# Kernel tuning notes

Hardware: AMD Instinct MI355X
Metric: run time of the kernel (lower is better)

Reference implementation:

```python
import jax, jax.numpy as jnp
import numpy as np

DIM = 2048
NUM_HEADS = 4  # hardcoded in RetNext.__init__
HEAD_DIM = DIM // NUM_HEADS
B, T = 4, 4096


def setup_inputs() -> dict:
    key = jax.random.key(0)
    ks = jax.random.split(key, 7)
    s = 1.0 / np.sqrt(DIM)  # roughly nn.Linear init scale
    return {
        "x": jax.random.normal(ks[0], (B, T, DIM), dtype=jnp.float32),
        "Wk": jax.random.normal(ks[1], (DIM, DIM), dtype=jnp.float32) * s,
        "bk": jax.random.normal(ks[2], (DIM,), dtype=jnp.float32) * s,
        "Wq": jax.random.normal(ks[3], (DIM, DIM), dtype=jnp.float32) * s,
        "bq": jax.random.normal(ks[4], (DIM,), dtype=jnp.float32) * s,
        "Wv": jax.random.normal(ks[5], (DIM, DIM), dtype=jnp.float32) * s,
        "bv": jax.random.normal(ks[6], (DIM,), dtype=jnp.float32) * s,
    }


def reference(x, Wk, bk, Wq, bq, Wv, bv):
    bsz, seq_len, _ = x.shape
    # nn.Linear: y = x @ W.T + b
    k = x @ Wk.T + bk
    q = x @ Wq.T + bq
    v = x @ Wv.T + bv
    # (b, s, h, d) -> (b, h, s, d)
    k = k.reshape(bsz, seq_len, NUM_HEADS, HEAD_DIM).transpose(0, 2, 1, 3)
    q = q.reshape(bsz, seq_len, NUM_HEADS, HEAD_DIM).transpose(0, 2, 1, 3)
    v = v.reshape(bsz, seq_len, NUM_HEADS, HEAD_DIM).transpose(0, 2, 1, 3)
    # states = k^T @ v : (b, h, d, d)
    states = jnp.einsum("bhsd,bhse->bhde", k, v)
    # out = q @ states : (b, h, s, d) -- returned WITHOUT reshape, as in the source
    out = jnp.einsum("bhsd,bhde->bhse", q, states)
    return out
```

## Files before the change

### kernel.cpp

```cpp
#include <hip/hip_runtime.h>
#include <cstdint>
#include <cstddef>

typedef __bf16 bf16;
typedef bf16 bf16x8 __attribute__((ext_vector_type(8)));
typedef float f32x4 __attribute__((ext_vector_type(4)));
typedef unsigned short u16;
typedef u16 u16x4 __attribute__((ext_vector_type(4)));
typedef u16 u16x8 __attribute__((ext_vector_type(8)));

__device__ __forceinline__ u16 f2bf(float f) {
    uint32_t u = __builtin_bit_cast(uint32_t, f);
    u += 0x7FFFu + ((u >> 16) & 1u);
    return (u16)(u >> 16);
}

#define AS1C(p) ((const __attribute__((address_space(1))) uint32_t*)(p))
#define AS3(p)  ((__attribute__((address_space(3))) uint32_t*)(p))

__device__ __forceinline__ void gemm_core(const bf16* __restrict__ Ablk,
                                          const bf16* __restrict__ Btblk,
                                          int lda, int ldb, int K,
                                          f32x4 acc[4][4])
{
    __shared__ bf16 lA[4096];
    __shared__ bf16 lB[4096];

    const int tid  = threadIdx.x;
    const int wave = tid >> 6;
    const int lane = tid & 63;
    const int lrow = lane >> 2;
    const int kcol = (lane & 3) << 3;

    const bf16* ga0 = Ablk  + (size_t)(wave * 32 + lrow) * lda + kcol;
    const bf16* ga1 = ga0 + (size_t)16 * lda;
    const bf16* gb0 = Btblk + (size_t)(wave * 32 + lrow) * ldb + kcol;
    const bf16* gb1 = gb0 + (size_t)16 * ldb;
    bf16* la0 = &lA[wave * 1024];
    bf16* la1 = &lA[wave * 1024 + 512];
    bf16* lb0 = &lB[wave * 1024];
    bf16* lb1 = &lB[wave * 1024 + 512];

    const int wm    = (wave >> 1) * 64;
    const int wn    = (wave & 1) * 64;
    const int col16 = lane & 15;
    const int quad  = lane >> 4;
    const bf16* pa = &lA[(wm + col16) * 32 + quad * 8];
    const bf16* pb = &lB[(wn + col16) * 32 + quad * 8];

    for (int kb = 0; kb < K; kb += 32) {
        __builtin_amdgcn_global_load_lds(AS1C(ga0 + kb), AS3(la0), 16, 0, 0);
        __builtin_amdgcn_global_load_lds(AS1C(ga1 + kb), AS3(la1), 16, 0, 0);
        __builtin_amdgcn_global_load_lds(AS1C(gb0 + kb), AS3(lb0), 16, 0, 0);
        __builtin_amdgcn_global_load_lds(AS1C(gb1 + kb), AS3(lb1), 16, 0, 0);
        __syncthreads();

        bf16x8 av[4], bv[4];
        #pragma unroll
        for (int i = 0; i < 4; ++i) av[i] = *(const bf16x8*)(pa + i * 512);
        #pragma unroll
        for (int i = 0; i < 4; ++i) bv[i] = *(const bf16x8*)(pb + i * 512);

        #pragma unroll
        for (int mi = 0; mi < 4; ++mi)
            #pragma unroll
            for (int ni = 0; ni < 4; ++ni)
                acc[mi][ni] = __builtin_amdgcn_mfma_f32_16x16x32_bf16(
                    av[mi], bv[ni], acc[mi][ni], 0, 0, 0);
        __syncthreads();
    }
}

__global__ __launch_bounds__(256) void cast_bf16(const float* __restrict__ src,
                                                 u16* __restrict__ dst, int n8)
{
    int i = blockIdx.x * 256 + threadIdx.x;
    if (i >= n8) return;
    const float4* s = (const float4*)src + (size_t)i * 2;
    float4 f0 = s[0], f1 = s[1];
    u16x8 o;
    o[0] = f2bf(f0.x); o[1] = f2bf(f0.y); o[2] = f2bf(f0.z); o[3] = f2bf(f0.w);
    o[4] = f2bf(f1.x); o[5] = f2bf(f1.y); o[6] = f2bf(f1.z); o[7] = f2bf(f1.w);
    *((u16x8*)dst + i) = o;
}

__global__ __launch_bounds__(256) void gemm_qkv(
    const bf16* __restrict__ xb,
    const bf16* __restrict__ Wkb, const bf16* __restrict__ Wqb, const bf16* __restrict__ Wvb,
    const float* __restrict__ bk, const float* __restrict__ bq, const float* __restrict__ bv,
    u16* __restrict__ qout, u16* __restrict__ kT, u16* __restrict__ vT)
{
    const int bx = blockIdx.x;
    const int by = blockIdx.y;
    const int region = by >> 4;
    const int nloc = (by & 15) << 7;

    const bf16* W     = (region == 0) ? Wkb : (region == 1) ? Wqb : Wvb;
    const float* bias = (region == 0) ? bk  : (region == 1) ? bq  : bv;

    f32x4 acc[4][4] = {};
    gemm_core(xb + (size_t)bx * 128 * 2048, W + (size_t)nloc * 2048,
              2048, 2048, 2048, acc);

    const int lane = threadIdx.x & 63, wave = threadIdx.x >> 6;
    const int wm = (wave >> 1) * 64, wn = (wave & 1) * 64;
    const int col16 = lane & 15, quad = lane >> 4;

    if (region == 1) {
        #pragma unroll
        for (int mi = 0; mi < 4; ++mi) {
            int row = bx * 128 + wm + mi * 16 + quad * 4;
            #pragma unroll
            for (int ni = 0; ni < 4; ++ni) {
                int col = nloc + wn + ni * 16 + col16;
                float b = bias[col];
                #pragma unroll
                for (int r = 0; r < 4; ++r)
                    qout[(size_t)(row + r) * 2048 + col] = f2bf(acc[mi][ni][r] + b);
            }
        }
    } else {
        u16* T = (region == 0) ? kT : vT;
        const int b_ = bx >> 5;
        const int h_ = nloc >> 9;
        const int bh = b_ * 4 + h_;
        #pragma unroll
        for (int mi = 0; mi < 4; ++mi) {
            int s = ((bx & 31) * 128) + wm + mi * 16 + quad * 4;
            #pragma unroll
            for (int ni = 0; ni < 4; ++ni) {
                int fcol = nloc + wn + ni * 16 + col16;
                int d = fcol & 511;
                float b = bias[fcol];
                u16x4 p;
                #pragma unroll
                for (int r = 0; r < 4; ++r) p[r] = f2bf(acc[mi][ni][r] + b);
                *(u16x4*)&T[((size_t)(bh * 512 + d)) * 4096 + s] = p;
            }
        }
    }
}

__global__ __launch_bounds__(256) void gemm_states(
    const u16* __restrict__ vT, const u16* __restrict__ kT, u16* __restrict__ ST)
{
    const int bh = blockIdx.z;
    const int m0 = blockIdx.x * 128;
    const int n0 = blockIdx.y * 128;

    f32x4 acc[4][4] = {};
    gemm_core((const bf16*)vT + (size_t)bh * 2097152 + (size_t)m0 * 4096,
              (const bf16*)kT + (size_t)bh * 2097152 + (size_t)n0 * 4096,
              4096, 4096, 4096, acc);

    const int lane = threadIdx.x & 63, wave = threadIdx.x >> 6;
    const int wm = (wave >> 1) * 64, wn = (wave & 1) * 64;
    const int col16 = lane & 15, quad = lane >> 4;
    #pragma unroll
    for (int mi = 0; mi < 4; ++mi) {
        int row = m0 + wm + mi * 16 + quad * 4;
        #pragma unroll
        for (int ni = 0; ni < 4; ++ni) {
            int col = n0 + wn + ni * 16 + col16;
            #pragma unroll
            for (int r = 0; r < 4; ++r)
                ST[(size_t)bh * 262144 + (size_t)(row + r) * 512 + col] =
                    f2bf(acc[mi][ni][r]);
        }
    }
}

__global__ __launch_bounds__(256) void gemm_out(
    const u16* __restrict__ qb, const u16* __restrict__ ST, float* __restrict__ out)
{
    const int bh = blockIdx.z;
    const int b_ = bh >> 2, h_ = bh & 3;
    const int m0 = blockIdx.x * 128;
    const int n0 = blockIdx.y * 128;

    f32x4 acc[4][4] = {};
    gemm_core((const bf16*)qb + ((size_t)(b_ * 4096 + m0)) * 2048 + h_ * 512,
              (const bf16*)ST + (size_t)bh * 262144 + (size_t)n0 * 512,
              2048, 512, 512, acc);

    const int lane = threadIdx.x & 63, wave = threadIdx.x >> 6;
    const int wm = (wave >> 1) * 64, wn = (wave & 1) * 64;
    const int col16 = lane & 15, quad = lane >> 4;
    #pragma unroll
    for (int mi = 0; mi < 4; ++mi) {
        int row = m0 + wm + mi * 16 + quad * 4;
        #pragma unroll
        for (int ni = 0; ni < 4; ++ni) {
            int col = n0 + wn + ni * 16 + col16;
            #pragma unroll
            for (int r = 0; r < 4; ++r)
                out[(size_t)bh * 2097152 + (size_t)(row + r) * 512 + col] =
                    acc[mi][ni][r];
        }
    }
}

extern "C" void kernel_launch(void* const* d_in, const int* in_sizes, int n_in,
                              void* d_out, int out_size, void* d_ws, size_t ws_size,
                              hipStream_t stream)
{
    (void)in_sizes; (void)n_in; (void)out_size; (void)ws_size;
    const float* x  = (const float*)d_in[0];
    const float* Wk = (const float*)d_in[1];
    const float* bk = (const float*)d_in[2];
    const float* Wq = (const float*)d_in[3];
    const float* bq = (const float*)d_in[4];
    const float* Wv = (const float*)d_in[5];
    const float* bv = (const float*)d_in[6];
    float* out = (float*)d_out;

    u16* ws  = (u16*)d_ws;
    u16* xb  = ws;
    u16* Wkb = ws  + 33554432;
    u16* Wqb = Wkb + 4194304;
    u16* Wvb = Wqb + 4194304;
    u16* qb  = Wvb + 4194304;
    u16* kT  = qb  + 33554432;
    u16* vT  = kT  + 33554432;
    u16* ST  = vT  + 33554432;

    cast_bf16<<<16384, 256, 0, stream>>>(x,  xb,  4194304);
    cast_bf16<<<2048,  256, 0, stream>>>(Wk, Wkb, 524288);
    cast_bf16<<<2048,  256, 0, stream>>>(Wq, Wqb, 524288);
    cast_bf16<<<2048,  256, 0, stream>>>(Wv, Wvb, 524288);

    gemm_qkv<<<dim3(128, 48), 256, 0, stream>>>(
        (const bf16*)xb, (const bf16*)Wkb, (const bf16*)Wqb, (const bf16*)Wvb,
        bk, bq, bv, qb, kT, vT);

    gemm_states<<<dim3(4, 4, 16), 256, 0, stream>>>(vT, kT, ST);

    gemm_out<<<dim3(32, 4, 16), 256, 0, stream>>>(qb, ST, out);
}
```

Before: 979.7 us.

## Rewrite QKV GEMM with 256x256 tiles, triple-buffered LDS and swizzled layout

The QKV projection GEMM gets its own main loop. It uses 256x256 tiles on 512 threads and a three-stage LDS ring buffer fed by global_load_lds, so the loads for the tile two steps ahead overlap the MFMAs on the current one. An XOR swizzle is applied to the LDS layout to avoid bank conflicts, and s_setprio wraps the MFMA bursts. The aim is to remove the per-iteration load/compute serialisation and the low reuse of the old 128x128 single-buffered core, which costs more registers (128 accumulator floats per thread) and 96KB of LDS per block.

```diff
diff --git a/kernel.cpp b/kernel.cpp
--- a/kernel.cpp
+++ b/kernel.cpp
@@ -17,6 +17,7 @@
 
 #define AS1C(p) ((const __attribute__((address_space(1))) uint32_t*)(p))
 #define AS3(p)  ((__attribute__((address_space(3))) uint32_t*)(p))
+#define MFMA16  __builtin_amdgcn_mfma_f32_16x16x32_bf16
 
 __device__ __forceinline__ void gemm_core(const bf16* __restrict__ Ablk,
                                           const bf16* __restrict__ Btblk,
@@ -65,8 +66,7 @@
         for (int mi = 0; mi < 4; ++mi)
             #pragma unroll
             for (int ni = 0; ni < 4; ++ni)
-                acc[mi][ni] = __builtin_amdgcn_mfma_f32_16x16x32_bf16(
-                    av[mi], bv[ni], acc[mi][ni], 0, 0, 0);
+                acc[mi][ni] = MFMA16(av[mi], bv[ni], acc[mi][ni], 0, 0, 0);
         __syncthreads();
     }
 }
@@ -84,32 +84,147 @@
     *((u16x8*)dst + i) = o;
 }
 
-__global__ __launch_bounds__(256) void gemm_qkv(
+__global__ __launch_bounds__(512, 2) void gemm_qkv(
     const bf16* __restrict__ xb,
     const bf16* __restrict__ Wkb, const bf16* __restrict__ Wqb, const bf16* __restrict__ Wvb,
     const float* __restrict__ bk, const float* __restrict__ bq, const float* __restrict__ bv,
     u16* __restrict__ qout, u16* __restrict__ kT, u16* __restrict__ vT)
 {
+    __shared__ bf16 smem[49152];
+    char* sm = (char*)smem;
+
     const int bx = blockIdx.x;
     const int by = blockIdx.y;
-    const int region = by >> 4;
-    const int nloc = (by & 15) << 7;
+    const int region = by >> 3;
+    const int nloc = (by & 7) << 8;
 
     const bf16* W     = (region == 0) ? Wkb : (region == 1) ? Wqb : Wvb;
     const float* bias = (region == 0) ? bk  : (region == 1) ? bq  : bv;
 
-    f32x4 acc[4][4] = {};
-    gemm_core(xb + (size_t)bx * 128 * 2048, W + (size_t)nloc * 2048,
-              2048, 2048, 2048, acc);
-
-    const int lane = threadIdx.x & 63, wave = threadIdx.x >> 6;
-    const int wm = (wave >> 1) * 64, wn = (wave & 1) * 64;
-    const int col16 = lane & 15, quad = lane >> 4;
+    const bf16* Ablk = xb + (size_t)bx * 256 * 2048;
+    const bf16* Bblk = W  + (size_t)nloc * 2048;
+    const int lda = 2048, ldb = 2048;
+    const int NT = 2048 / 32;
+
+    const int tid  = threadIdx.x;
+    const int wave = tid >> 6;
+    const int lane = tid & 63;
+    const int col16 = lane & 15;
+    const int quad  = lane >> 4;
+    const int wm = (wave >> 2) * 128;
+    const int wn = (wave & 3) * 64;
+
+    const int P0 = tid * 16;
+    const int T0 = P0 ^ ((P0 >> 2) & 0x70) ^ ((P0 >> 4) & 0x10);
+    const int r0 = T0 >> 6;
+    const int ce = (T0 & 63) >> 1;
+    const bf16* gA0 = Ablk + (size_t)r0 * lda + ce;
+    const bf16* gA1 = Ablk + (size_t)(r0 + 128) * lda + ce;
+    const bf16* gB0 = Bblk + (size_t)r0 * ldb + ce;
+    const bf16* gB1 = Bblk + (size_t)(r0 + 128) * ldb + ce;
+    const int dA0 = wave * 1024;
+    const int dA1 = 8192  + wave * 1024;
+    const int dB0 = 16384 + wave * 1024;
+    const int dB1 = 24576 + wave * 1024;
+
+    int offA[8], offB[4];
+    #pragma unroll
+    for (int mi = 0; mi < 8; ++mi) {
+        int T = (wm + mi * 16 + col16) * 64 + quad * 16;
+        offA[mi] = T ^ ((T >> 2) & 0x70);
+    }
+    #pragma unroll
+    for (int ni = 0; ni < 4; ++ni) {
+        int T = (wn + ni * 16 + col16) * 64 + quad * 16;
+        offB[ni] = 16384 + (T ^ ((T >> 2) & 0x70));
+    }
+
+    f32x4 acc[8][4] = {};
+
+#define GLD(src, dst) __builtin_amdgcn_global_load_lds(AS1C(src), AS3(sm + (dst)), 16, 0, 0)
+
+    GLD(gA0,      0 + dA0); GLD(gB0,      0 + dB0);
+    GLD(gA1,      0 + dA1); GLD(gB1,      0 + dB1);
+    GLD(gA0 + 32, 32768 + dA0); GLD(gB0 + 32, 32768 + dB0);
+    GLD(gA1 + 32, 32768 + dA1); GLD(gB1 + 32, 32768 + dB1);
+    asm volatile("s_waitcnt vmcnt(4)" ::: "memory");
+    __builtin_amdgcn_s_barrier();
+    asm volatile("" ::: "memory");
+
+    int buf = 0, sb = 2;
+    for (int t = 0; t < NT; ++t) {
+        const int  bb  = buf * 32768;
+        const int  sbb = sb  * 32768;
+        const int  kb  = (t + 2) * 32;
+        const bool st  = (t + 2) < NT;
+
+        bf16x8 a0 = *(const bf16x8*)(sm + bb + offA[0]);
+        bf16x8 a1 = *(const bf16x8*)(sm + bb + offA[1]);
+        bf16x8 a2 = *(const bf16x8*)(sm + bb + offA[2]);
+        bf16x8 a3 = *(const bf16x8*)(sm + bb + offA[3]);
+        bf16x8 b0 = *(const bf16x8*)(sm + bb + offB[0]);
+        bf16x8 b1 = *(const bf16x8*)(sm + bb + offB[1]);
+        bf16x8 b2 = *(const bf16x8*)(sm + bb + offB[2]);
+        bf16x8 b3 = *(const bf16x8*)(sm + bb + offB[3]);
+        if (st) { GLD(gA0 + kb, sbb + dA0); GLD(gB0 + kb, sbb + dB0); }
+        __builtin_amdgcn_s_setprio(1);
+        acc[0][0] = MFMA16(a0, b0, acc[0][0], 0, 0, 0);
+        acc[0][1] = MFMA16(a0, b1, acc[0][1], 0, 0, 0);
+        acc[0][2] = MFMA16(a0, b2, acc[0][2], 0, 0, 0);
+        acc[0][3] = MFMA16(a0, b3, acc[0][3], 0, 0, 0);
+        acc[1][0] = MFMA16(a1, b0, acc[1][0], 0, 0, 0);
+        acc[1][1] = MFMA16(a1, b1, acc[1][1], 0, 0, 0);
+        acc[1][2] = MFMA16(a1, b2, acc[1][2], 0, 0, 0);
+        acc[1][3] = MFMA16(a1, b3, acc[1][3], 0, 0, 0);
+        acc[2][0] = MFMA16(a2, b0, acc[2][0], 0, 0, 0);
+        acc[2][1] = MFMA16(a2, b1, acc[2][1], 0, 0, 0);
+        acc[2][2] = MFMA16(a2, b2, acc[2][2], 0, 0, 0);
+        acc[2][3] = MFMA16(a2, b3, acc[2][3], 0, 0, 0);
+        acc[3][0] = MFMA16(a3, b0, acc[3][0], 0, 0, 0);
+        acc[3][1] = MFMA16(a3, b1, acc[3][1], 0, 0, 0);
+        acc[3][2] = MFMA16(a3, b2, acc[3][2], 0, 0, 0);
+        acc[3][3] = MFMA16(a3, b3, acc[3][3], 0, 0, 0);
+        __builtin_amdgcn_s_setprio(0);
+        __builtin_amdgcn_s_barrier();
+        asm volatile("" ::: "memory");
+
+        bf16x8 a4 = *(const bf16x8*)(sm + bb + offA[4]);
+        bf16x8 a5 = *(const bf16x8*)(sm + bb + offA[5]);
+        bf16x8 a6 = *(const bf16x8*)(sm + bb + offA[6]);
+        bf16x8 a7 = *(const bf16x8*)(sm + bb + offA[7]);
+        if (st) { GLD(gA1 + kb, sbb + dA1); GLD(gB1 + kb, sbb + dB1); }
+        if (st) { asm volatile("s_waitcnt vmcnt(4)" ::: "memory"); }
+        else    { asm volatile("s_waitcnt vmcnt(0)" ::: "memory"); }
+        __builtin_amdgcn_s_setprio(1);
+        acc[4][0] = MFMA16(a4, b0, acc[4][0], 0, 0, 0);
+        acc[4][1] = MFMA16(a4, b1, acc[4][1], 0, 0, 0);
+        acc[4][2] = MFMA16(a4, b2, acc[4][2], 0, 0, 0);
+        acc[4][3] = MFMA16(a4, b3, acc[4][3], 0, 0, 0);
+        acc[5][0] = MFMA16(a5, b0, acc[5][0], 0, 0, 0);
+        acc[5][1] = MFMA16(a5, b1, acc[5][1], 0, 0, 0);
+        acc[5][2] = MFMA16(a5, b2, acc[5][2], 0, 0, 0);
+        acc[5][3] = MFMA16(a5, b3, acc[5][3], 0, 0, 0);
+        acc[6][0] = MFMA16(a6, b0, acc[6][0], 0, 0, 0);
+        acc[6][1] = MFMA16(a6, b1, acc[6][1], 0, 0, 0);
+        acc[6][2] = MFMA16(a6, b2, acc[6][2], 0, 0, 0);
+        acc[6][3] = MFMA16(a6, b3, acc[6][3], 0, 0, 0);
+        acc[7][0] = MFMA16(a7, b0, acc[7][0], 0, 0, 0);
+        acc[7][1] = MFMA16(a7, b1, acc[7][1], 0, 0, 0);
+        acc[7][2] = MFMA16(a7, b2, acc[7][2], 0, 0, 0);
+        acc[7][3] = MFMA16(a7, b3, acc[7][3], 0, 0, 0);
+        __builtin_amdgcn_s_setprio(0);
+        __builtin_amdgcn_s_barrier();
+        asm volatile("" ::: "memory");
+
+        buf = (buf == 2) ? 0 : buf + 1;
+        sb  = (sb  == 2) ? 0 : sb  + 1;
+    }
+#undef GLD
 
     if (region == 1) {
         #pragma unroll
-        for (int mi = 0; mi < 4; ++mi) {
-            int row = bx * 128 + wm + mi * 16 + quad * 4;
+        for (int mi = 0; mi < 8; ++mi) {
+            int row = bx * 256 + wm + mi * 16 + quad * 4;
             #pragma unroll
             for (int ni = 0; ni < 4; ++ni) {
                 int col = nloc + wn + ni * 16 + col16;
@@ -121,12 +236,12 @@
         }
     } else {
         u16* T = (region == 0) ? kT : vT;
-        const int b_ = bx >> 5;
+        const int b_ = bx >> 4;
         const int h_ = nloc >> 9;
         const int bh = b_ * 4 + h_;
         #pragma unroll
-        for (int mi = 0; mi < 4; ++mi) {
-            int s = ((bx & 31) * 128) + wm + mi * 16 + quad * 4;
+        for (int mi = 0; mi < 8; ++mi) {
+            int s = ((bx & 15) * 256) + wm + mi * 16 + quad * 4;
             #pragma unroll
             for (int ni = 0; ni < 4; ++ni) {
                 int fcol = nloc + wn + ni * 16 + col16;
@@ -229,7 +344,7 @@
     cast_bf16<<<2048,  256, 0, stream>>>(Wq, Wqb, 524288);
     cast_bf16<<<2048,  256, 0, stream>>>(Wv, Wvb, 524288);
 
-    gemm_qkv<<<dim3(128, 48), 256, 0, stream>>>(
+    gemm_qkv<<<dim3(64, 24), 512, 0, stream>>>(
         (const bf16*)xb, (const bf16*)Wkb, (const bf16*)Wqb, (const bf16*)Wvb,
         bk, bq, bv, qb, kT, vT);
 
```

Result: faster. 818.2 us (-16.5%).
